# Performance work log

Hardware: AMD Instinct MI355X
Metric: run time of the kernel (lower is better)

Reference implementation:

```python
import jax, jax.numpy as jnp
import numpy as np

N0, N1, N2, N3 = 200000, 100000, 50000, 25000
E0, E1, E2 = 1600000, 800000, 400000
IN_DIM, HID = 16, 128


def setup_inputs() -> dict:
    key = jax.random.key(0)
    ks = jax.random.split(key, 12)
    inp = {
        "features": jax.random.normal(ks[0], (N0, IN_DIM), jnp.float32),
        "W_init": jax.random.normal(ks[1], (IN_DIM, HID), jnp.float32) / np.sqrt(IN_DIM),
        "b_init": jnp.zeros((HID,), jnp.float32),
        "W_self": jax.random.normal(ks[2], (HID, HID), jnp.float32) / np.sqrt(HID),
        "b_self": jnp.zeros((HID,), jnp.float32),
        "W_neigh": jax.random.normal(ks[3], (HID, HID), jnp.float32) / np.sqrt(HID),
        "b_neigh": jnp.zeros((HID,), jnp.float32),
        "src0": jax.random.randint(ks[4], (E0,), 0, N0, jnp.int32),
        "dst0": jax.random.randint(ks[5], (E0,), 0, N1, jnp.int32),
        "src1": jax.random.randint(ks[6], (E1,), 0, N1, jnp.int32),
        "dst1": jax.random.randint(ks[7], (E1,), 0, N2, jnp.int32),
        "src2": jax.random.randint(ks[8], (E2,), 0, N2, jnp.int32),
        "dst2": jax.random.randint(ks[9], (E2,), 0, N3, jnp.int32),
        "n1": N1, "n2": N2, "n3": N3,
    }
    return inp


def _mean_agg(h_src, src, dst, n_out):
    # gather messages along edges, segment-mean into dst nodes
    msg = h_src[src]                                             # [E, HID]
    agg = jax.ops.segment_sum(msg, dst, num_segments=n_out)      # [n_out, HID]
    cnt = jax.ops.segment_sum(jnp.ones_like(dst, jnp.float32), dst, num_segments=n_out)
    return agg / jnp.maximum(cnt, 1.0)[:, None]


def reference(features, W_init, b_init, W_self, b_self, W_neigh, b_neigh,
              src0, dst0, src1, dst1, src2, dst2, n1, n2, n3):
    # h = activation(fc_init(features))
    h = jax.nn.relu(features @ W_init + b_init)                  # [N0, HID]
    blocks = [(src0, dst0, n1), (src1, dst1, n2), (src2, dst2, n3)]
    depth = len(blocks)
    for i, (src, dst, n_out) in enumerate(blocks):
        h_neigh = _mean_agg(h, src, dst, n_out)
        # SAGEConv mean, combine_type='sum': fc_self(h_dst) + fc_neigh(mean_neigh)
        h = (h[:n_out] @ W_self + b_self) + (h_neigh @ W_neigh + b_neigh)
        if i != depth - 1:
            h = jax.nn.relu(h)
    return h                                                     # [N3, HID]
```

## Files before the change

### kernel.cpp

```cpp
#include <hip/hip_runtime.h>

#define HID 128
#define CAP 64
#define SHB 9
#define NCB0 196
#define NCB1 98
#define NCB2 49
#define SUB 32
#define CS 384
#define CB 9000
#define TILE 2048

typedef __attribute__((ext_vector_type(2))) _Float16 h2v;
typedef __attribute__((ext_vector_type(8))) _Float16 f16x8;
typedef __attribute__((ext_vector_type(4))) float f32x4;


__device__ __forceinline__ void acc8(float* s, uint4 u) {
    union { uint4 u; h2v p[4]; } w; w.u = u;
#pragma unroll
    for (int q = 0; q < 4; q++) {
        s[2 * q]     += (float)w.p[q][0];
        s[2 * q + 1] += (float)w.p[q][1];
    }
}

__device__ __forceinline__ uint4 mean_chunk(const _Float16* __restrict__ h,
                                            const int* __restrict__ sl, int deg, int c) {
    float s[8] = {0.f, 0.f, 0.f, 0.f, 0.f, 0.f, 0.f, 0.f};
    int e = 0;
    if (deg >= 8) {
        int idx[8];
#pragma unroll
        for (int k = 0; k < 8; k++) idx[k] = sl[k];
        int nxt = 8;
        while (nxt + 8 <= deg) {
            uint4 R[8];
#pragma unroll
            for (int k = 0; k < 8; k++)
                R[k] = *(const uint4*)(h + (size_t)idx[k] * HID + c * 8);
            int nidx[8];
#pragma unroll
            for (int k = 0; k < 8; k++) nidx[k] = sl[nxt + k];
#pragma unroll
            for (int k = 0; k < 8; k++) acc8(s, R[k]);
#pragma unroll
            for (int k = 0; k < 8; k++) idx[k] = nidx[k];
            nxt += 8;
        }
        uint4 R[8];
#pragma unroll
        for (int k = 0; k < 8; k++)
            R[k] = *(const uint4*)(h + (size_t)idx[k] * HID + c * 8);
#pragma unroll
        for (int k = 0; k < 8; k++) acc8(s, R[k]);
        e = nxt;
    }
    if (e + 4 <= deg) {
        uint4 R[4];
#pragma unroll
        for (int k = 0; k < 4; k++)
            R[k] = *(const uint4*)(h + (size_t)sl[e + k] * HID + c * 8);
#pragma unroll
        for (int k = 0; k < 4; k++) acc8(s, R[k]);
        e += 4;
    }
    for (; e < deg; e++)
        acc8(s, *(const uint4*)(h + (size_t)sl[e] * HID + c * 8));
    float inv = 1.0f / (float)max(deg, 1);
    union { uint4 u; h2v p[4]; } mo;
#pragma unroll
    for (int q = 0; q < 4; q++)
        mo.p[q] = (h2v){(_Float16)(s[2 * q] * inv), (_Float16)(s[2 * q + 1] * inv)};
    return mo.u;
}

__device__ __forceinline__ void bin_dev(
        const int* __restrict__ src, const int* __restrict__ dst, int E,
        int lb, int nblk, int* __restrict__ buf, int* __restrict__ cur, int ncb,
        int* hist, int* gbase) {
    const int sub = lb & (SUB - 1);
    const int ntile = (E + TILE - 1) / TILE;
    for (int t = lb; t < ntile; t += nblk) {
        const int base = t * TILE;
        const int n = min(TILE, E - base);
        for (int i = threadIdx.x; i < ncb; i += 256) hist[i] = 0;
        __syncthreads();
        int eb[8], er[8], ee[8];
#pragma unroll
        for (int k = 0; k < 8; k++) {
            int idx = k * 256 + threadIdx.x;
            eb[k] = -1;
            if (idx < n) {
                int d = dst[base + idx], s = src[base + idx];
                int bb = d >> SHB;
                eb[k] = bb;
                ee[k] = ((d & 511) << 18) | s;
                er[k] = atomicAdd(&hist[bb], 1);
            }
        }
        __syncthreads();
        for (int i = threadIdx.x; i < ncb; i += 256)
            gbase[i] = atomicAdd(&cur[i * SUB + sub], hist[i]);
        __syncthreads();
#pragma unroll
        for (int k = 0; k < 8; k++) {
            if (eb[k] >= 0) {
                int pos = gbase[eb[k]] + er[k];
                if (pos < CS) buf[((size_t)eb[k] * SUB + sub) * CS + pos] = ee[k];
            }
        }
        __syncthreads();
    }
}

__device__ __forceinline__ void refine_dev(
        const int* __restrict__ buf, const int* __restrict__ cur,
        int* __restrict__ csr, int* __restrict__ off, int* __restrict__ cnt,
        int N, int bb, int* hist, int* loff, int* wsum) {
    const int tid = threadIdx.x;
    hist[tid] = 0;
    __syncthreads();
#pragma unroll 4
    for (int j = 0; j < SUB; j++) {
        const int mj = min(cur[bb * SUB + j], CS);
        const int* __restrict__ seg = buf + ((size_t)bb * SUB + j) * CS;
        for (int i = tid; i < mj; i += 512)
            atomicAdd(&hist[((unsigned)seg[i]) >> 18], 1);
    }
    __syncthreads();
    int v = hist[tid];
    int lane = tid & 63;
    int incl = v;
#pragma unroll
    for (int d = 1; d < 64; d <<= 1) {
        int up = __shfl_up(incl, d, 64);
        if (lane >= d) incl += up;
    }
    if (lane == 63) wsum[tid >> 6] = incl;
    __syncthreads();
    if (tid == 0) {
        int acc = 0;
#pragma unroll
        for (int i = 0; i < 8; i++) { int w = wsum[i]; wsum[i] = acc; acc += w; }
    }
    __syncthreads();
    int base = wsum[tid >> 6] + (incl - v);
    loff[tid] = base;
    const int node = (bb << SHB) + tid;
    if (node < N) {
        off[node] = bb * CB + base;
        cnt[node] = min(v, max(0, CB - base));
    }
    __syncthreads();
    hist[tid] = 0;
    __syncthreads();
#pragma unroll 4
    for (int j = 0; j < SUB; j++) {
        const int mj = min(cur[bb * SUB + j], CS);
        const int* __restrict__ seg = buf + ((size_t)bb * SUB + j) * CS;
        for (int i = tid; i < mj; i += 512) {
            int e = seg[i];
            int dl = ((unsigned)e) >> 18;
            int p = atomicAdd(&hist[dl], 1);
            int pos = loff[dl] + p;
            if (pos < CB) csr[(size_t)bb * CB + pos] = e & 0x3FFFF;
        }
    }
}

__global__ __launch_bounds__(256) void bin_all(
        const int* __restrict__ src0, const int* __restrict__ dst0, int E0,
        const int* __restrict__ src1, const int* __restrict__ dst1, int E1,
        const int* __restrict__ src2, const int* __restrict__ dst2, int E2,
        int* __restrict__ gcur,
        int* __restrict__ buf0, int* __restrict__ buf1, int* __restrict__ buf2,
        const float* __restrict__ Wself, const float* __restrict__ bself,
        const float* __restrict__ Wneigh, const float* __restrict__ bneigh,
        _Float16* __restrict__ Bpack, float* __restrict__ biasp,
        int nb0, int nb1, int nb2) {
    __shared__ int hist[NCB0];
    __shared__ int gbase[NCB0];
    const int b = blockIdx.x;
    const int nbTot = nb0 + nb1 + nb2;
    if (b >= nbTot) {
        const int pb = b - nbTot;
        const int s  = pb >> 1;
        const int cc = pb & 1;
        const int tid  = threadIdx.x;
        const int wave = tid >> 6;
        const int lane = tid & 63;
        const int ln15 = lane & 15;
        const int quad = lane >> 4;
        const int n = (wave * 2 + cc) * 16 + ln15;
        if (pb == 0 && tid < HID) biasp[tid] = bself[tid] + bneigh[tid];
        f16x8 v;
#pragma unroll
        for (int jj = 0; jj < 8; jj++) {
            int k = s * 32 + quad * 8 + jj;
            float w = (k < HID) ? Wself[k * HID + n] : Wneigh[(k - HID) * HID + n];
            v[jj] = (_Float16)w;
        }
        *(f16x8*)(Bpack + ((size_t)(s * 2 + cc) * 256 + tid) * 8) = v;
        return;
    }
    if (b < nb0)
        bin_dev(src0, dst0, E0, b, nb0, buf0, gcur, NCB0, hist, gbase);
    else if (b < nb0 + nb1)
        bin_dev(src1, dst1, E1, b - nb0, nb1, buf1, gcur + NCB0 * SUB, NCB1, hist, gbase);
    else
        bin_dev(src2, dst2, E2, b - nb0 - nb1, nb2, buf2, gcur + (NCB0 + NCB1) * SUB, NCB2, hist, gbase);
}

__global__ __launch_bounds__(512) void refine_h0(
        const int* __restrict__ buf0, const int* __restrict__ buf1, const int* __restrict__ buf2,
        const int* __restrict__ gcur,
        int N1v, int N2v, int N3v, int nRef,
        int* __restrict__ csr0, int* __restrict__ off0, int* __restrict__ cnt0,
        int* __restrict__ csr1, int* __restrict__ off1, int* __restrict__ cnt1,
        int* __restrict__ csr2, int* __restrict__ off2, int* __restrict__ cnt2,
        const float* __restrict__ feat, const float* __restrict__ W_init,
        const float* __restrict__ b_init, _Float16* __restrict__ h0, int M, int nh0) {
    __shared__ int hist[512];
    __shared__ int loff[512];
    __shared__ int wsum[8];
    const int tid = threadIdx.x;
    if (blockIdx.x < (unsigned)nRef) {
        const int gb = blockIdx.x;
        if (gb < NCB0)
            refine_dev(buf0, gcur, csr0, off0, cnt0, N1v, gb, hist, loff, wsum);
        else if (gb < NCB0 + NCB1)
            refine_dev(buf1, gcur + NCB0 * SUB, csr1, off1, cnt1, N2v, gb - NCB0,
                       hist, loff, wsum);
        else
            refine_dev(buf2, gcur + (NCB0 + NCB1) * SUB, csr2, off2, cnt2, N3v,
                       gb - NCB0 - NCB1, hist, loff, wsum);
        return;
    }
    const int hb   = blockIdx.x - nRef;
    const int sb   = tid >> 8;
    const int t    = tid & 255;
    const int lane = t & 63;
    const int wave = t >> 6;
    const int ln15 = lane & 15;
    const int quad = lane >> 4;

    f16x8 Bf[2];
    float bias[2];
#pragma unroll
    for (int cc = 0; cc < 2; cc++) {
        int n = (wave * 2 + cc) * 16 + ln15;
        bias[cc] = b_init[n];
        f16x8 b;
#pragma unroll
        for (int jj = 0; jj < 8; jj++) {
            int k = quad * 8 + jj;
            b[jj] = (k < 16) ? (_Float16)W_init[k * HID + n] : (_Float16)0.f;
        }
        Bf[cc] = b;
    }

    for (int row0 = (hb * 2 + sb) * 16; row0 < M; row0 += nh0 * 32) {
        const int arow = row0 + ln15;
        f16x8 A = {0, 0, 0, 0, 0, 0, 0, 0};
        if (arow < M && quad < 2) {
            const float* p = feat + (size_t)arow * 16 + quad * 8;
            float4 v0 = *(const float4*)p;
            float4 v1 = *(const float4*)(p + 4);
            A[0] = (_Float16)v0.x; A[1] = (_Float16)v0.y;
            A[2] = (_Float16)v0.z; A[3] = (_Float16)v0.w;
            A[4] = (_Float16)v1.x; A[5] = (_Float16)v1.y;
            A[6] = (_Float16)v1.z; A[7] = (_Float16)v1.w;
        }
        f32x4 acc0 = {0.f, 0.f, 0.f, 0.f};
        f32x4 acc1 = {0.f, 0.f, 0.f, 0.f};
        acc0 = __builtin_amdgcn_mfma_f32_16x16x32_f16(A, Bf[0], acc0, 0, 0, 0);
        acc1 = __builtin_amdgcn_mfma_f32_16x16x32_f16(A, Bf[1], acc1, 0, 0, 0);
#pragma unroll
        for (int cc = 0; cc < 2; cc++) {
            int col = (wave * 2 + cc) * 16 + ln15;
            f32x4 acc = cc ? acc1 : acc0;
#pragma unroll
            for (int r = 0; r < 4; r++) {
                int row = row0 + quad * 4 + r;
                if (row < M)
                    h0[(size_t)row * HID + col] = (_Float16)fmaxf(acc[r] + bias[cc], 0.f);
            }
        }
    }
}

__global__ __launch_bounds__(256) void gather_mean_p(
        const _Float16* __restrict__ h,
        const int* __restrict__ csr,
        const int* __restrict__ off,
        const int* __restrict__ cnt,
        _Float16* __restrict__ Xm,
        int n_out, int nblk) {
    const int g = threadIdx.x >> 4;
    const int c = threadIdx.x & 15;
    const int ntile = (n_out + 15) >> 4;
    for (int t = blockIdx.x; t < ntile; t += nblk) {
        const int node = t * 16 + g;
        if (node < n_out) {
            int deg = min(cnt[node], CAP);
            uint4 mo = mean_chunk(h, csr + off[node], deg, c);
            *(uint4*)(Xm + (size_t)node * HID + c * 8) = mo;
        }
    }
}

template <bool RELU, typename OutT>
__global__ __launch_bounds__(256) void mfma_combine2(
        const _Float16* Hself, const _Float16* __restrict__ Xm,
        const _Float16* __restrict__ Bpack, const float* __restrict__ biasp,
        OutT* out, int M) {
    const int tid  = threadIdx.x;
    const int lane = tid & 63;
    const int wave = tid >> 6;
    const int ln15 = lane & 15;
    const int quad = lane >> 4;

    f16x8 Bf[2][8];
    float bias[2];
#pragma unroll
    for (int cc = 0; cc < 2; cc++) {
        bias[cc] = biasp[(wave * 2 + cc) * 16 + ln15];
#pragma unroll
        for (int s = 0; s < 8; s++)
            Bf[cc][s] = *(const f16x8*)(Bpack + ((size_t)(s * 2 + cc) * 256 + tid) * 8);
    }

    for (int row0 = blockIdx.x * 16; row0 < M; row0 += gridDim.x * 16) {
        const int arow = row0 + ln15;
        const bool inb = arow < M;
        const _Float16* aps = Hself + (size_t)arow * HID + quad * 8;
        const _Float16* apm = Xm    + (size_t)arow * HID + quad * 8;
        f32x4 acc0 = {0.f, 0.f, 0.f, 0.f};
        f32x4 acc1 = {0.f, 0.f, 0.f, 0.f};
#pragma unroll
        for (int s = 0; s < 8; s++) {
            f16x8 A;
            if (inb) A = (s < 4) ? *(const f16x8*)(aps + s * 32)
                                 : *(const f16x8*)(apm + (s - 4) * 32);
            else     A = (f16x8){0, 0, 0, 0, 0, 0, 0, 0};
            acc0 = __builtin_amdgcn_mfma_f32_16x16x32_f16(A, Bf[0][s], acc0, 0, 0, 0);
            acc1 = __builtin_amdgcn_mfma_f32_16x16x32_f16(A, Bf[1][s], acc1, 0, 0, 0);
        }
        __syncthreads();
#pragma unroll
        for (int cc = 0; cc < 2; cc++) {
            int col = (wave * 2 + cc) * 16 + ln15;
            f32x4 acc = cc ? acc1 : acc0;
#pragma unroll
            for (int r = 0; r < 4; r++) {
                int row = row0 + quad * 4 + r;
                if (row < M) {
                    float v = acc[r] + bias[cc];
                    if (RELU) v = fmaxf(v, 0.f);
                    out[(size_t)row * HID + col] = (OutT)v;
                }
            }
        }
    }
}

extern "C" void kernel_launch(void* const* d_in, const int* in_sizes, int n_in,
                              void* d_out, int out_size, void* d_ws, size_t ws_size,
                              hipStream_t stream) {
    const float* feat    = (const float*)d_in[0];
    const float* W_init  = (const float*)d_in[1];
    const float* b_init  = (const float*)d_in[2];
    const float* W_self  = (const float*)d_in[3];
    const float* b_self  = (const float*)d_in[4];
    const float* W_neigh = (const float*)d_in[5];
    const float* b_neigh = (const float*)d_in[6];
    const int* src0 = (const int*)d_in[7];
    const int* dst0 = (const int*)d_in[8];
    const int* src1 = (const int*)d_in[9];
    const int* dst1 = (const int*)d_in[10];
    const int* src2 = (const int*)d_in[11];
    const int* dst2 = (const int*)d_in[12];

    const int N0 = in_sizes[0] / 16;
    const int E0 = in_sizes[7];
    const int E1 = in_sizes[9];
    const int E2 = in_sizes[11];
    const int N1 = 100000, N2 = 50000, N3 = 25000;

    _Float16* h  = (_Float16*)d_ws;
    _Float16* Xm = h + (size_t)N0 * HID;
    int* csr0 = (int*)(Xm + (size_t)N1 * HID);
    int* csr1 = csr0 + (size_t)NCB0 * CB;
    int* csr2 = csr1 + (size_t)NCB1 * CB;
    int* off0 = csr2 + (size_t)NCB2 * CB;
    int* off1 = off0 + N1;
    int* off2 = off1 + N2;
    int* cnt0 = off2 + N3;
    int* cnt1 = cnt0 + N1;
    int* cnt2 = cnt1 + N2;
    _Float16* Bpack = (_Float16*)(cnt2 + N3);
    float* biasp = (float*)(Bpack + 16 * 256 * 8);
    int* gcur = (int*)(biasp + HID);
    int* buf0 = gcur + (NCB0 + NCB1 + NCB2) * SUB;
    int* buf1 = buf0 + (size_t)NCB0 * SUB * CS;
    int* buf2 = buf1 + (size_t)NCB1 * SUB * CS;

    hipMemsetAsync(gcur, 0, (size_t)(NCB0 + NCB1 + NCB2) * SUB * sizeof(int), stream);

    const int nb0 = 768, nb1 = 384, nb2 = 192;
    bin_all<<<nb0 + nb1 + nb2 + 16, 256, 0, stream>>>(
        src0, dst0, E0, src1, dst1, E1, src2, dst2, E2,
        gcur, buf0, buf1, buf2,
        W_self, b_self, W_neigh, b_neigh, Bpack, biasp,
        nb0, nb1, nb2);

    const int nRef = NCB0 + NCB1 + NCB2, nh0 = 3072;
    refine_h0<<<nRef + nh0, 512, 0, stream>>>(
        buf0, buf1, buf2, gcur, N1, N2, N3, nRef,
        csr0, off0, cnt0, csr1, off1, cnt1, csr2, off2, cnt2,
        feat, W_init, b_init, h, N0, nh0);

    gather_mean_p<<<2048, 256, 0, stream>>>(h, csr0, off0, cnt0, Xm, N1, 2048);
    mfma_combine2<true, _Float16><<<min((N1 + 15) / 16, 2048), 256, 0, stream>>>(
        h, Xm, Bpack, biasp, h, N1);
    gather_mean_p<<<2048, 256, 0, stream>>>(h, csr1, off1, cnt1, Xm, N2, 2048);
    mfma_combine2<true, _Float16><<<min((N2 + 15) / 16, 2048), 256, 0, stream>>>(
        h, Xm, Bpack, biasp, h, N2);
    {
        int g = (N3 + 15) / 16;
        gather_mean_p<<<g, 256, 0, stream>>>(h, csr2, off2, cnt2, Xm, N3, g);
    }
    mfma_combine2<false, float><<<min((N3 + 15) / 16, 2048), 256, 0, stream>>>(
        h, Xm, Bpack, biasp, (float*)d_out, N3);
}
```

Measured before the change: 352.6 us.

## Replace atomic-cursor binning with per-tile count tables and split h0 across kernels

Binning now has each tile write its edges into a fixed-capacity slot per (bucket, tile) and record the count in a table. This removes the global atomic cursors and the memset that zeroed them. Refine reads the per-tile counts and walks a flat span. The h0 init GEMM is split by rows, with the first 100k rows computed in the binning kernel and the rest in the refine kernel to balance work. Bin buffers are moved to alias the Xm workspace. Fixed per-tile capacities (CSEG) can silently drop edges if a bucket overflows within a tile.

```diff
diff --git a/kernel.cpp b/kernel.cpp
--- a/kernel.cpp
+++ b/kernel.cpp
@@ -6,10 +6,12 @@
 #define NCB0 196
 #define NCB1 98
 #define NCB2 49
-#define SUB 32
-#define CS 384
 #define CB 9000
-#define TILE 2048
+#define TL0 8192
+#define TL12 4096
+#define CSEG0 94
+#define CSEG1 94
+#define CSEG2 160
 
 typedef __attribute__((ext_vector_type(2))) _Float16 h2v;
 typedef __attribute__((ext_vector_type(8))) _Float16 f16x8;
@@ -75,58 +77,45 @@
     return mo.u;
 }
 
+template <int TL, int CSEG>
 __device__ __forceinline__ void bin_dev(
         const int* __restrict__ src, const int* __restrict__ dst, int E,
-        int lb, int nblk, int* __restrict__ buf, int* __restrict__ cur, int ncb,
-        int* hist, int* gbase) {
-    const int sub = lb & (SUB - 1);
-    const int ntile = (E + TILE - 1) / TILE;
-    for (int t = lb; t < ntile; t += nblk) {
-        const int base = t * TILE;
-        const int n = min(TILE, E - base);
-        for (int i = threadIdx.x; i < ncb; i += 256) hist[i] = 0;
-        __syncthreads();
-        int eb[8], er[8], ee[8];
-#pragma unroll
-        for (int k = 0; k < 8; k++) {
-            int idx = k * 256 + threadIdx.x;
-            eb[k] = -1;
-            if (idx < n) {
-                int d = dst[base + idx], s = src[base + idx];
-                int bb = d >> SHB;
-                eb[k] = bb;
-                ee[k] = ((d & 511) << 18) | s;
-                er[k] = atomicAdd(&hist[bb], 1);
-            }
-        }
-        __syncthreads();
-        for (int i = threadIdx.x; i < ncb; i += 256)
-            gbase[i] = atomicAdd(&cur[i * SUB + sub], hist[i]);
-        __syncthreads();
-#pragma unroll
-        for (int k = 0; k < 8; k++) {
-            if (eb[k] >= 0) {
-                int pos = gbase[eb[k]] + er[k];
-                if (pos < CS) buf[((size_t)eb[k] * SUB + sub) * CS + pos] = ee[k];
-            }
-        }
-        __syncthreads();
-    }
-}
-
+        int t, int NT, int* __restrict__ buf, int* __restrict__ cbt, int ncb,
+        int* hist) {
+    const int base = t * TL;
+    const int n = min(TL, E - base);
+    for (int i = threadIdx.x; i < ncb; i += 256) hist[i] = 0;
+    __syncthreads();
+    const int EPT = TL / 256;
+#pragma unroll 4
+    for (int k = 0; k < EPT; k++) {
+        int idx = k * 256 + threadIdx.x;
+        if (idx < n) {
+            int d = dst[base + idx], s = src[base + idx];
+            int bb = d >> SHB;
+            int r = atomicAdd(&hist[bb], 1);
+            if (r < CSEG) buf[((size_t)bb * NT + t) * CSEG + r] = ((d & 511) << 18) | s;
+        }
+    }
+    __syncthreads();
+    for (int i = threadIdx.x; i < ncb; i += 256) cbt[(size_t)i * NT + t] = hist[i];
+}
+
+template <int CSEG>
 __device__ __forceinline__ void refine_dev(
-        const int* __restrict__ buf, const int* __restrict__ cur,
+        const int* __restrict__ buf, const int* __restrict__ cbt, int NT,
         int* __restrict__ csr, int* __restrict__ off, int* __restrict__ cnt,
-        int N, int bb, int* hist, int* loff, int* wsum) {
+        int N, int bb, int* hist, int* loff, int* wsum, int* mt) {
     const int tid = threadIdx.x;
+    for (int i = tid; i < NT; i += 512) mt[i] = min(cbt[(size_t)bb * NT + i], CSEG);
     hist[tid] = 0;
     __syncthreads();
-#pragma unroll 4
-    for (int j = 0; j < SUB; j++) {
-        const int mj = min(cur[bb * SUB + j], CS);
-        const int* __restrict__ seg = buf + ((size_t)bb * SUB + j) * CS;
-        for (int i = tid; i < mj; i += 512)
-            atomicAdd(&hist[((unsigned)seg[i]) >> 18], 1);
+    const int span = NT * CSEG;
+    const int* __restrict__ seg0 = buf + (size_t)bb * NT * CSEG;
+    for (int i = tid; i < span; i += 512) {
+        int t = i / CSEG, r = i - t * CSEG;
+        if (r < mt[t])
+            atomicAdd(&hist[((unsigned)seg0[(size_t)t * CSEG + r]) >> 18], 1);
     }
     __syncthreads();
     int v = hist[tid];
@@ -155,12 +144,10 @@
     __syncthreads();
     hist[tid] = 0;
     __syncthreads();
-#pragma unroll 4
-    for (int j = 0; j < SUB; j++) {
-        const int mj = min(cur[bb * SUB + j], CS);
-        const int* __restrict__ seg = buf + ((size_t)bb * SUB + j) * CS;
-        for (int i = tid; i < mj; i += 512) {
-            int e = seg[i];
+    for (int i = tid; i < span; i += 512) {
+        int t = i / CSEG, r = i - t * CSEG;
+        if (r < mt[t]) {
+            int e = seg0[(size_t)t * CSEG + r];
             int dl = ((unsigned)e) >> 18;
             int p = atomicAdd(&hist[dl], 1);
             int pos = loff[dl] + p;
@@ -169,31 +156,86 @@
     }
 }
 
-__global__ __launch_bounds__(256) void bin_all(
+__device__ __forceinline__ void h0_tile(
+        const float* __restrict__ feat, const f16x8* Bf, const float* bias,
+        _Float16* __restrict__ h0, int row0, int M,
+        int ln15, int quad, int wave) {
+    const int arow = row0 + ln15;
+    f16x8 A = {0, 0, 0, 0, 0, 0, 0, 0};
+    if (arow < M && quad < 2) {
+        const float* p = feat + (size_t)arow * 16 + quad * 8;
+        float4 v0 = *(const float4*)p;
+        float4 v1 = *(const float4*)(p + 4);
+        A[0] = (_Float16)v0.x; A[1] = (_Float16)v0.y;
+        A[2] = (_Float16)v0.z; A[3] = (_Float16)v0.w;
+        A[4] = (_Float16)v1.x; A[5] = (_Float16)v1.y;
+        A[6] = (_Float16)v1.z; A[7] = (_Float16)v1.w;
+    }
+    f32x4 acc0 = {0.f, 0.f, 0.f, 0.f};
+    f32x4 acc1 = {0.f, 0.f, 0.f, 0.f};
+    acc0 = __builtin_amdgcn_mfma_f32_16x16x32_f16(A, Bf[0], acc0, 0, 0, 0);
+    acc1 = __builtin_amdgcn_mfma_f32_16x16x32_f16(A, Bf[1], acc1, 0, 0, 0);
+#pragma unroll
+    for (int cc = 0; cc < 2; cc++) {
+        int col = (wave * 2 + cc) * 16 + ln15;
+        f32x4 acc = cc ? acc1 : acc0;
+#pragma unroll
+        for (int r = 0; r < 4; r++) {
+            int row = row0 + quad * 4 + r;
+            if (row < M)
+                h0[(size_t)row * HID + col] = (_Float16)fmaxf(acc[r] + bias[cc], 0.f);
+        }
+    }
+}
+
+__device__ __forceinline__ void h0_loadB(
+        const float* __restrict__ W_init, const float* __restrict__ b_init,
+        f16x8* Bf, float* bias, int ln15, int quad, int wave) {
+#pragma unroll
+    for (int cc = 0; cc < 2; cc++) {
+        int n = (wave * 2 + cc) * 16 + ln15;
+        bias[cc] = b_init[n];
+        f16x8 b;
+#pragma unroll
+        for (int jj = 0; jj < 8; jj++) {
+            int k = quad * 8 + jj;
+            b[jj] = (k < 16) ? (_Float16)W_init[k * HID + n] : (_Float16)0.f;
+        }
+        Bf[cc] = b;
+    }
+}
+
+__global__ __launch_bounds__(256) void bin_pack_h0(
         const int* __restrict__ src0, const int* __restrict__ dst0, int E0,
         const int* __restrict__ src1, const int* __restrict__ dst1, int E1,
         const int* __restrict__ src2, const int* __restrict__ dst2, int E2,
-        int* __restrict__ gcur,
         int* __restrict__ buf0, int* __restrict__ buf1, int* __restrict__ buf2,
+        int* __restrict__ cbt0, int* __restrict__ cbt1, int* __restrict__ cbt2,
+        int NT0, int NT1, int NT2,
         const float* __restrict__ Wself, const float* __restrict__ bself,
         const float* __restrict__ Wneigh, const float* __restrict__ bneigh,
         _Float16* __restrict__ Bpack, float* __restrict__ biasp,
-        int nb0, int nb1, int nb2) {
+        const float* __restrict__ feat, const float* __restrict__ W_init,
+        const float* __restrict__ b_init, _Float16* __restrict__ h0,
+        int M, int rowSplit, int nh0) {
     __shared__ int hist[NCB0];
-    __shared__ int gbase[NCB0];
-    const int b = blockIdx.x;
-    const int nbTot = nb0 + nb1 + nb2;
-    if (b >= nbTot) {
-        const int pb = b - nbTot;
-        const int s  = pb >> 1;
-        const int cc = pb & 1;
-        const int tid  = threadIdx.x;
-        const int wave = tid >> 6;
-        const int lane = tid & 63;
-        const int ln15 = lane & 15;
-        const int quad = lane >> 4;
+    int b = blockIdx.x;
+    if (b < NT0) { bin_dev<TL0, CSEG0>(src0, dst0, E0, b, NT0, buf0, cbt0, NCB0, hist); return; }
+    b -= NT0;
+    if (b < NT1) { bin_dev<TL12, CSEG1>(src1, dst1, E1, b, NT1, buf1, cbt1, NCB1, hist); return; }
+    b -= NT1;
+    if (b < NT2) { bin_dev<TL12, CSEG2>(src2, dst2, E2, b, NT2, buf2, cbt2, NCB2, hist); return; }
+    b -= NT2;
+    const int tid  = threadIdx.x;
+    const int lane = tid & 63;
+    const int wave = tid >> 6;
+    const int ln15 = lane & 15;
+    const int quad = lane >> 4;
+    if (b < 16) {
+        const int s  = b >> 1;
+        const int cc = b & 1;
         const int n = (wave * 2 + cc) * 16 + ln15;
-        if (pb == 0 && tid < HID) biasp[tid] = bself[tid] + bneigh[tid];
+        if (b == 0 && tid < HID) biasp[tid] = bself[tid] + bneigh[tid];
         f16x8 v;
 #pragma unroll
         for (int jj = 0; jj < 8; jj++) {
@@ -204,37 +246,39 @@
         *(f16x8*)(Bpack + ((size_t)(s * 2 + cc) * 256 + tid) * 8) = v;
         return;
     }
-    if (b < nb0)
-        bin_dev(src0, dst0, E0, b, nb0, buf0, gcur, NCB0, hist, gbase);
-    else if (b < nb0 + nb1)
-        bin_dev(src1, dst1, E1, b - nb0, nb1, buf1, gcur + NCB0 * SUB, NCB1, hist, gbase);
-    else
-        bin_dev(src2, dst2, E2, b - nb0 - nb1, nb2, buf2, gcur + (NCB0 + NCB1) * SUB, NCB2, hist, gbase);
+    b -= 16;
+    f16x8 Bf[2];
+    float bias[2];
+    h0_loadB(W_init, b_init, Bf, bias, ln15, quad, wave);
+    for (int row0 = b * 16; row0 < rowSplit; row0 += nh0 * 16)
+        h0_tile(feat, Bf, bias, h0, row0, M, ln15, quad, wave);
 }
 
 __global__ __launch_bounds__(512) void refine_h0(
         const int* __restrict__ buf0, const int* __restrict__ buf1, const int* __restrict__ buf2,
-        const int* __restrict__ gcur,
-        int N1v, int N2v, int N3v, int nRef,
+        const int* __restrict__ cbt0, const int* __restrict__ cbt1, const int* __restrict__ cbt2,
+        int NT0, int NT1, int NT2,
+        int N1v, int N2v, int N3v,
         int* __restrict__ csr0, int* __restrict__ off0, int* __restrict__ cnt0,
         int* __restrict__ csr1, int* __restrict__ off1, int* __restrict__ cnt1,
         int* __restrict__ csr2, int* __restrict__ off2, int* __restrict__ cnt2,
         const float* __restrict__ feat, const float* __restrict__ W_init,
-        const float* __restrict__ b_init, _Float16* __restrict__ h0, int M, int nh0) {
+        const float* __restrict__ b_init, _Float16* __restrict__ h0,
+        int M, int rowSplit, int nh0) {
     __shared__ int hist[512];
     __shared__ int loff[512];
     __shared__ int wsum[8];
+    __shared__ int mt[256];
+    const int nRef = NCB0 + NCB1 + NCB2;
     const int tid = threadIdx.x;
     if (blockIdx.x < (unsigned)nRef) {
         const int gb = blockIdx.x;
         if (gb < NCB0)
-            refine_dev(buf0, gcur, csr0, off0, cnt0, N1v, gb, hist, loff, wsum);
+            refine_dev<CSEG0>(buf0, cbt0, NT0, csr0, off0, cnt0, N1v, gb, hist, loff, wsum, mt);
         else if (gb < NCB0 + NCB1)
-            refine_dev(buf1, gcur + NCB0 * SUB, csr1, off1, cnt1, N2v, gb - NCB0,
-                       hist, loff, wsum);
+            refine_dev<CSEG1>(buf1, cbt1, NT1, csr1, off1, cnt1, N2v, gb - NCB0, hist, loff, wsum, mt);
         else
-            refine_dev(buf2, gcur + (NCB0 + NCB1) * SUB, csr2, off2, cnt2, N3v,
-                       gb - NCB0 - NCB1, hist, loff, wsum);
+            refine_dev<CSEG2>(buf2, cbt2, NT2, csr2, off2, cnt2, N3v, gb - NCB0 - NCB1, hist, loff, wsum, mt);
         return;
     }
     const int hb   = blockIdx.x - nRef;
@@ -244,50 +288,11 @@
     const int wave = t >> 6;
     const int ln15 = lane & 15;
     const int quad = lane >> 4;
-
     f16x8 Bf[2];
     float bias[2];
-#pragma unroll
-    for (int cc = 0; cc < 2; cc++) {
-        int n = (wave * 2 + cc) * 16 + ln15;
-        bias[cc] = b_init[n];
-        f16x8 b;
-#pragma unroll
-        for (int jj = 0; jj < 8; jj++) {
-            int k = quad * 8 + jj;
-            b[jj] = (k < 16) ? (_Float16)W_init[k * HID + n] : (_Float16)0.f;
-        }
-        Bf[cc] = b;
-    }
-
-    for (int row0 = (hb * 2 + sb) * 16; row0 < M; row0 += nh0 * 32) {
-        const int arow = row0 + ln15;
-        f16x8 A = {0, 0, 0, 0, 0, 0, 0, 0};
-        if (arow < M && quad < 2) {
-            const float* p = feat + (size_t)arow * 16 + quad * 8;
-            float4 v0 = *(const float4*)p;
-            float4 v1 = *(const float4*)(p + 4);
-            A[0] = (_Float16)v0.x; A[1] = (_Float16)v0.y;
-            A[2] = (_Float16)v0.z; A[3] = (_Float16)v0.w;
-            A[4] = (_Float16)v1.x; A[5] = (_Float16)v1.y;
-            A[6] = (_Float16)v1.z; A[7] = (_Float16)v1.w;
-        }
-        f32x4 acc0 = {0.f, 0.f, 0.f, 0.f};
-        f32x4 acc1 = {0.f, 0.f, 0.f, 0.f};
-        acc0 = __builtin_amdgcn_mfma_f32_16x16x32_f16(A, Bf[0], acc0, 0, 0, 0);
-        acc1 = __builtin_amdgcn_mfma_f32_16x16x32_f16(A, Bf[1], acc1, 0, 0, 0);
-#pragma unroll
-        for (int cc = 0; cc < 2; cc++) {
-            int col = (wave * 2 + cc) * 16 + ln15;
-            f32x4 acc = cc ? acc1 : acc0;
-#pragma unroll
-            for (int r = 0; r < 4; r++) {
-                int row = row0 + quad * 4 + r;
-                if (row < M)
-                    h0[(size_t)row * HID + col] = (_Float16)fmaxf(acc[r] + bias[cc], 0.f);
-            }
-        }
-    }
+    h0_loadB(W_init, b_init, Bf, bias, ln15, quad, wave);
+    for (int row0 = rowSplit + (hb * 2 + sb) * 16; row0 < M; row0 += nh0 * 32)
+        h0_tile(feat, Bf, bias, h0, row0, M, ln15, quad, wave);
 }
 
 __global__ __launch_bounds__(256) void gather_mean_p(
@@ -388,8 +393,15 @@
     const int E2 = in_sizes[11];
     const int N1 = 100000, N2 = 50000, N3 = 25000;
 
+    const int NT0 = (E0 + TL0 - 1) / TL0;
+    const int NT1 = (E1 + TL12 - 1) / TL12;
+    const int NT2 = (E2 + TL12 - 1) / TL12;
+
     _Float16* h  = (_Float16*)d_ws;
     _Float16* Xm = h + (size_t)N0 * HID;
+    int* buf0 = (int*)Xm;
+    int* buf1 = buf0 + (size_t)NCB0 * NT0 * CSEG0;
+    int* buf2 = buf1 + (size_t)NCB1 * NT1 * CSEG1;
     int* csr0 = (int*)(Xm + (size_t)N1 * HID);
     int* csr1 = csr0 + (size_t)NCB0 * CB;
     int* csr2 = csr1 + (size_t)NCB1 * CB;
@@ -399,27 +411,27 @@
     int* cnt0 = off2 + N3;
     int* cnt1 = cnt0 + N1;
     int* cnt2 = cnt1 + N2;
-    _Float16* Bpack = (_Float16*)(cnt2 + N3);
+    int* cbt0 = cnt2 + N3;
+    int* cbt1 = cbt0 + (size_t)NCB0 * NT0;
+    int* cbt2 = cbt1 + (size_t)NCB1 * NT1;
+    _Float16* Bpack = (_Float16*)(cbt2 + (size_t)NCB2 * NT2);
     float* biasp = (float*)(Bpack + 16 * 256 * 8);
-    int* gcur = (int*)(biasp + HID);
-    int* buf0 = gcur + (NCB0 + NCB1 + NCB2) * SUB;
-    int* buf1 = buf0 + (size_t)NCB0 * SUB * CS;
-    int* buf2 = buf1 + (size_t)NCB1 * SUB * CS;
-
-    hipMemsetAsync(gcur, 0, (size_t)(NCB0 + NCB1 + NCB2) * SUB * sizeof(int), stream);
-
-    const int nb0 = 768, nb1 = 384, nb2 = 192;
-    bin_all<<<nb0 + nb1 + nb2 + 16, 256, 0, stream>>>(
+
+    const int rowSplit = 100000;
+
+    const int nh0a = 1600;
+    bin_pack_h0<<<NT0 + NT1 + NT2 + 16 + nh0a, 256, 0, stream>>>(
         src0, dst0, E0, src1, dst1, E1, src2, dst2, E2,
-        gcur, buf0, buf1, buf2,
+        buf0, buf1, buf2, cbt0, cbt1, cbt2, NT0, NT1, NT2,
         W_self, b_self, W_neigh, b_neigh, Bpack, biasp,
-        nb0, nb1, nb2);
-
-    const int nRef = NCB0 + NCB1 + NCB2, nh0 = 3072;
-    refine_h0<<<nRef + nh0, 512, 0, stream>>>(
-        buf0, buf1, buf2, gcur, N1, N2, N3, nRef,
+        feat, W_init, b_init, h, N0, rowSplit, nh0a);
+
+    const int nRef = NCB0 + NCB1 + NCB2, nh0b = 2000;
+    refine_h0<<<nRef + nh0b, 512, 0, stream>>>(
+        buf0, buf1, buf2, cbt0, cbt1, cbt2, NT0, NT1, NT2,
+        N1, N2, N3,
         csr0, off0, cnt0, csr1, off1, cnt1, csr2, off2, cnt2,
-        feat, W_init, b_init, h, N0, nh0);
+        feat, W_init, b_init, h, N0, rowSplit, nh0b);
 
     gather_mean_p<<<2048, 256, 0, stream>>>(h, csr0, off0, cnt0, Xm, N1, 2048);
     mfma_combine2<true, _Float16><<<min((N1 + 15) / 16, 2048), 256, 0, stream>>>(
```

Result: no change. 358.0 us (+1.5%).

## Fuse neighbor-mean gather with MFMA combine for layers 1 and 2

Applied to the files above, without the earlier changes.

Adds a gather_combine kernel that computes each 16-node tile's neighbor mean into shared memory and then runs the self+neighbor MFMA combine in the same block. Layers 1 and 2 use it, with ping-pong buffers (Xm reused as layer-1 output) so the fused kernel never reads rows it is overwriting. This removes the Xm round trip through global memory and two kernel launches. The cost is a block-wide barrier between gather and matmul, which may reduce overlap.

```diff
diff --git a/kernel.cpp b/kernel.cpp
--- a/kernel.cpp
+++ b/kernel.cpp
@@ -312,7 +312,7 @@
 
 template <bool RELU, typename OutT>
 __global__ __launch_bounds__(256) void mfma_combine2(
-        const _Float16* Hself, const _Float16* __restrict__ Xm,
+        const _Float16* Hself, const _Float16* Xm,
         const _Float16* __restrict__ Bpack, const float* __restrict__ biasp,
         OutT* out, int M) {
     const int tid  = threadIdx.x;
@@ -362,6 +362,79 @@
                 }
             }
         }
+    }
+}
+
+template <bool RELU, typename OutT>
+__global__ __launch_bounds__(256) void gather_combine(
+        const _Float16* __restrict__ hin,
+        const int* __restrict__ csr, const int* __restrict__ off, const int* __restrict__ cnt,
+        const _Float16* __restrict__ Bpack, const float* __restrict__ biasp,
+        OutT* __restrict__ out, int M, int nblk) {
+    __shared__ uint4 Xt[16][17];
+    const int tid  = threadIdx.x;
+    const int lane = tid & 63;
+    const int wave = tid >> 6;
+    const int ln15 = lane & 15;
+    const int quad = lane >> 4;
+    const int g = tid >> 4;
+    const int c = tid & 15;
+
+    f16x8 Bf[2][8];
+    float bias[2];
+#pragma unroll
+    for (int cc = 0; cc < 2; cc++) {
+        bias[cc] = biasp[(wave * 2 + cc) * 16 + ln15];
+#pragma unroll
+        for (int s = 0; s < 8; s++)
+            Bf[cc][s] = *(const f16x8*)(Bpack + ((size_t)(s * 2 + cc) * 256 + tid) * 8);
+    }
+
+    for (int row0 = blockIdx.x * 16; row0 < M; row0 += nblk * 16) {
+        {
+            const int node = row0 + g;
+            uint4 mo = (uint4){0, 0, 0, 0};
+            if (node < M) {
+                int deg = min(cnt[node], CAP);
+                mo = mean_chunk(hin, csr + off[node], deg, c);
+            }
+            Xt[g][c] = mo;
+        }
+        __syncthreads();
+        {
+            const int arow = row0 + ln15;
+            const bool inb = arow < M;
+            const _Float16* aps = hin + (size_t)arow * HID + quad * 8;
+            f32x4 acc0 = {0.f, 0.f, 0.f, 0.f};
+            f32x4 acc1 = {0.f, 0.f, 0.f, 0.f};
+#pragma unroll
+            for (int s = 0; s < 8; s++) {
+                f16x8 A;
+                if (s < 4) {
+                    if (inb) A = *(const f16x8*)(aps + s * 32);
+                    else     A = (f16x8){0, 0, 0, 0, 0, 0, 0, 0};
+                } else {
+                    A = *(const f16x8*)&Xt[ln15][(s - 4) * 4 + quad];
+                }
+                acc0 = __builtin_amdgcn_mfma_f32_16x16x32_f16(A, Bf[0][s], acc0, 0, 0, 0);
+                acc1 = __builtin_amdgcn_mfma_f32_16x16x32_f16(A, Bf[1][s], acc1, 0, 0, 0);
+            }
+#pragma unroll
+            for (int cc = 0; cc < 2; cc++) {
+                int col = (wave * 2 + cc) * 16 + ln15;
+                f32x4 acc = cc ? acc1 : acc0;
+#pragma unroll
+                for (int r = 0; r < 4; r++) {
+                    int row = row0 + quad * 4 + r;
+                    if (row < M) {
+                        float v = acc[r] + bias[cc];
+                        if (RELU) v = fmaxf(v, 0.f);
+                        out[(size_t)row * HID + col] = (OutT)v;
+                    }
+                }
+            }
+        }
+        __syncthreads();
     }
 }
 
@@ -405,6 +478,8 @@
     int* buf0 = gcur + (NCB0 + NCB1 + NCB2) * SUB;
     int* buf1 = buf0 + (size_t)NCB0 * SUB * CS;
     int* buf2 = buf1 + (size_t)NCB1 * SUB * CS;
+    _Float16* hA = Xm;
+    _Float16* hB = h;
 
     hipMemsetAsync(gcur, 0, (size_t)(NCB0 + NCB1 + NCB2) * SUB * sizeof(int), stream);
 
@@ -423,14 +498,16 @@
 
     gather_mean_p<<<2048, 256, 0, stream>>>(h, csr0, off0, cnt0, Xm, N1, 2048);
     mfma_combine2<true, _Float16><<<min((N1 + 15) / 16, 2048), 256, 0, stream>>>(
-        h, Xm, Bpack, biasp, h, N1);
-    gather_mean_p<<<2048, 256, 0, stream>>>(h, csr1, off1, cnt1, Xm, N2, 2048);
-    mfma_combine2<true, _Float16><<<min((N2 + 15) / 16, 2048), 256, 0, stream>>>(
-        h, Xm, Bpack, biasp, h, N2);
+        h, Xm, Bpack, biasp, hA, N1);
+
     {
-        int g = (N3 + 15) / 16;
-        gather_mean_p<<<g, 256, 0, stream>>>(h, csr2, off2, cnt2, Xm, N3, g);
-    }
-    mfma_combine2<false, float><<<min((N3 + 15) / 16, 2048), 256, 0, stream>>>(
-        h, Xm, Bpack, biasp, (float*)d_out, N3);
-}
+        int g = min((N2 + 15) / 16, 1568);
+        gather_combine<true, _Float16><<<g, 256, 0, stream>>>(
+            hA, csr1, off1, cnt1, Bpack, biasp, hB, N2, g);
+    }
+    {
+        int g = min((N3 + 15) / 16, 1568);
+        gather_combine<false, float><<<g, 256, 0, stream>>>(
+            hB, csr2, off2, cnt2, Bpack, biasp, (float*)d_out, N3, g);
+    }
+}
```

Result: no change. 353.4 us (+0.2%).
